# Kernel optimization log

Hardware: AMD Instinct MI355X
Metric: run time of the kernel (lower is better)

Reference implementation:

```python
import jax, jax.numpy as jnp
import numpy as np

B, HG, WG, D, NH, K = 4, 32, 32, 768, 12, 7
HD = D // NH  # 64


def _neigh_idx(H, W, k):
    # NATTEN semantics: 7x7 window centered at the query, shifted (clamped)
    # at borders so every query has exactly k*k neighbors.
    si = np.clip(np.arange(H) - k // 2, 0, H - k)  # [H] window row starts
    sj = np.clip(np.arange(W) - k // 2, 0, W - k)  # [W] window col starts
    ri = si[:, None] + np.arange(k)[None, :]       # [H, k]
    cj = sj[:, None] + np.arange(k)[None, :]       # [W, k]
    idx = ri[:, None, :, None] * W + cj[None, :, None, :]  # [H, W, k, k]
    return jnp.asarray(idx.reshape(H * W, k * k), dtype=jnp.int32)


def setup_inputs() -> dict:
    key = jax.random.key(0)
    ks = jax.random.split(key, 3)
    s = D ** -0.5
    return {
        "x": jax.random.normal(ks[0], (B, HG * WG, D), dtype=jnp.float32),
        "qkv_w": jax.random.normal(ks[1], (3 * D, D), dtype=jnp.float32) * s,
        "qkv_b": jnp.zeros((3 * D,), dtype=jnp.float32),
        "proj_w": jax.random.normal(ks[2], (D, D), dtype=jnp.float32) * s,
        "proj_b": jnp.zeros((D,), dtype=jnp.float32),
    }


def reference(x, qkv_w, qkv_b, proj_w, proj_b):
    b, n, d = x.shape  # n == HG*WG
    idx = _neigh_idx(HG, WG, K)  # [n, K*K] flat neighbor token indices

    qkv = x @ qkv_w.T + qkv_b                      # [b, n, 3d]
    q, k, v = jnp.split(qkv, 3, axis=-1)
    q = q.reshape(b, n, NH, HD) * (HD ** -0.5)     # [b, n, h, hd]
    k = k.reshape(b, n, NH, HD)
    v = v.reshape(b, n, NH, HD)

    kn = jnp.take(k, idx, axis=1)                  # [b, n, 49, h, hd]
    vn = jnp.take(v, idx, axis=1)                  # [b, n, 49, h, hd]

    scores = jnp.einsum('bnhd,bnkhd->bnhk', q, kn)  # [b, n, h, 49]
    attn = jax.nn.softmax(scores, axis=-1)
    out = jnp.einsum('bnhk,bnkhd->bnhd', attn, vn).reshape(b, n, d)
    return out @ proj_w.T + proj_b
```

## Files before the change

### kernel.cpp

```cpp
#include <hip/hip_runtime.h>


typedef __bf16 bf16x8 __attribute__((ext_vector_type(8)));
typedef short s16x4 __attribute__((ext_vector_type(4)));
typedef float f32x4 __attribute__((ext_vector_type(4)));

__device__ __forceinline__ unsigned short f2bf(float f) {
  unsigned u = __float_as_uint(f);
  u += 0x7fffu + ((u >> 16) & 1u);
  return (unsigned short)(u >> 16);
}

template <typename T>
__device__ __forceinline__ void gld_lds16(const T* g, T* l) {
  __builtin_amdgcn_global_load_lds((const __attribute__((address_space(1))) void*)g,
                                   (__attribute__((address_space(3))) void*)l, 16, 0, 0);
}

__global__ void cvt_kernel(const float* __restrict__ x, const float* __restrict__ w1,
                           const float* __restrict__ w2, unsigned short* __restrict__ xo,
                           unsigned short* __restrict__ w1o, unsigned short* __restrict__ w2o) {
  const int n1 = 4096 * 768 / 4;
  const int n2 = 2304 * 768 / 4;
  const int n3 = 768 * 768 / 4;
  int i = blockIdx.x * 256 + threadIdx.x;
  float4 v;
  unsigned short* dst;
  int o;
  if (i < n1) {
    o = i; v = ((const float4*)x)[o]; dst = xo;
  } else if (i < n1 + n2) {
    o = i - n1; v = ((const float4*)w1)[o]; dst = w1o;
  } else if (i < n1 + n2 + n3) {
    o = i - n1 - n2; v = ((const float4*)w2)[o]; dst = w2o;
  } else {
    return;
  }
  ushort4 r;
  r.x = f2bf(v.x); r.y = f2bf(v.y); r.z = f2bf(v.z); r.w = f2bf(v.w);
  ((ushort4*)dst)[o] = r;
}

template <int MT, int MODE>
__global__ __launch_bounds__(256) void gemm_bt(const unsigned short* __restrict__ A,
                                               const unsigned short* __restrict__ Bm,
                                               const float* __restrict__ bias,
                                               unsigned short* __restrict__ obf,
                                               unsigned short* __restrict__ vtout,
                                               float* __restrict__ of32,
                                               int M, int N, int Kd) {
  constexpr int BM = MT * 32;
  __shared__ __align__(16) unsigned short sA[2 * BM * 32];
  __shared__ __align__(16) unsigned short sB[2 * 128 * 32];
  const int tid = threadIdx.x;
  const int lane = tid & 63;
  const int wv = tid >> 6;
  const int m0 = blockIdx.y * BM, n0 = blockIdx.x * 128;
  const int wrow = (wv >> 1) * (MT * 16), wcol = (wv & 1) * 64;
  const int lr = lane & 15, lq = lane >> 4;

  f32x4 acc[MT][4] = {};

  const int ls = lane & 15, lc = lane >> 4;
  const unsigned short* pA  = A  + (size_t)(m0 + wv * 16 + ls) * Kd + lc * 8;
  const unsigned short* pA2 = A  + (size_t)(m0 + (wv + 4) * 16 + ls) * Kd + lc * 8;
  const unsigned short* pB  = Bm + (size_t)(n0 + wv * 16 + ls) * Kd + lc * 8;
  const unsigned short* pB2 = Bm + (size_t)(n0 + (wv + 4) * 16 + ls) * Kd + lc * 8;

  auto stage = [&](int it, int bsel) {
    const int k0 = it * 32;
    gld_lds16(pA + k0, sA + bsel * (BM * 32) + tid * 8);
    if (MT == 4) gld_lds16(pA2 + k0, sA + bsel * (BM * 32) + 2048 + tid * 8);
    gld_lds16(pB + k0, sB + bsel * 4096 + tid * 8);
    gld_lds16(pB2 + k0, sB + bsel * 4096 + 2048 + tid * 8);
  };

  const int nIter = Kd >> 5;
  stage(0, 0);
  __syncthreads();
  for (int it = 0; it < nIter; ++it) {
    const int cur = it & 1;
    if (it + 1 < nIter) stage(it + 1, cur ^ 1);
    const unsigned short* bA = sA + cur * (BM * 32);
    const unsigned short* bB = sB + cur * 4096;
    bf16x8 af[MT], bfr[4];
#pragma unroll
    for (int t = 0; t < MT; ++t)
      af[t] = *(const bf16x8*)(bA + ((wrow >> 4) + t) * 512 + lq * 128 + lr * 8);
#pragma unroll
    for (int t = 0; t < 4; ++t)
      bfr[t] = *(const bf16x8*)(bB + ((wcol >> 4) + t) * 512 + lq * 128 + lr * 8);
#pragma unroll
    for (int im = 0; im < MT; ++im)
#pragma unroll
      for (int in = 0; in < 4; ++in)
        acc[im][in] = __builtin_amdgcn_mfma_f32_16x16x32_bf16(af[im], bfr[in], acc[im][in], 0, 0, 0);
    __syncthreads();
  }

  if (MODE == 0) {
    const int sidx = n0 / 768;
    if (sidx == 2) {
#pragma unroll
      for (int im = 0; im < MT; ++im) {
#pragma unroll
        for (int in = 0; in < 4; ++in) {
          int gn = n0 + wcol + in * 16 + lr;
          int rem = gn - 1536;
          int hh = rem >> 6, dd = gn & 63;
          float bsv = bias[gn];
          int gm0 = m0 + wrow + im * 16 + lq * 4;
          ushort4 pk;
          pk.x = f2bf(acc[im][in][0] + bsv);
          pk.y = f2bf(acc[im][in][1] + bsv);
          pk.z = f2bf(acc[im][in][2] + bsv);
          pk.w = f2bf(acc[im][in][3] + bsv);
          *(ushort4*)(vtout + (size_t)(hh * 64 + dd) * 4096 + gm0) = pk;
        }
      }
    } else {
      const float scale = (sidx == 0) ? 0.18033688f : 1.0f;
#pragma unroll
      for (int im = 0; im < MT; ++im) {
#pragma unroll
        for (int in = 0; in < 4; ++in) {
          int gn = n0 + wcol + in * 16 + lr;
          int rem = gn - sidx * 768;
          int hh = rem >> 6, dd = gn & 63;
          float bsv = bias[gn];
#pragma unroll
          for (int r = 0; r < 4; ++r) {
            int gm = m0 + wrow + im * 16 + lq * 4 + r;
            float val = (acc[im][in][r] + bsv) * scale;
            obf[((size_t)(sidx * 12 + hh) * 4096 + gm) * 64 + dd] = f2bf(val);
          }
        }
      }
    }
  } else {
#pragma unroll
    for (int im = 0; im < MT; ++im) {
#pragma unroll
      for (int in = 0; in < 4; ++in) {
        int gn = n0 + wcol + in * 16 + lr;
        float bsv = bias[gn];
#pragma unroll
        for (int r = 0; r < 4; ++r) {
          int gm = m0 + wrow + im * 16 + lq * 4 + r;
          of32[(size_t)gm * N + gn] = acc[im][in][r] + bsv;
        }
      }
    }
  }
}

__global__ __launch_bounds__(256, 2) void natten_kernel(const unsigned short* __restrict__ qkvt,
                                                        unsigned short* __restrict__ aout) {
  __shared__ __align__(16) unsigned short sQ[64 * 64];
  __shared__ __align__(16) unsigned short sK[256 * 64];
  __shared__ __align__(16) unsigned short sVt[64 * 256];
  const int h = blockIdx.x, ip = blockIdx.y, b = blockIdx.z;
  const int i0 = ip * 2;
  const int tid = threadIdx.x, lane = tid & 63, wv = tid >> 6;
  const int lg = lane >> 4, lm = lane & 15;
  int si0 = i0 - 3; si0 = si0 < 0 ? 0 : si0; if (si0 > 25) si0 = 25;
  const int gb = b * 1024;
  const unsigned short* Qg = qkvt + ((size_t)h * 4096 + gb + i0 * 32) * 64;
  const unsigned short* Kg = qkvt + ((size_t)(12 + h) * 4096 + gb) * 64;
  const unsigned short* Vg = qkvt + (size_t)24 * 4096 * 64 + (size_t)h * 64 * 4096 + gb;

#pragma unroll
  for (int it = 0; it < 2; ++it) {
    int f = it * 256 + tid;
    int q = f >> 3, c16 = f & 7;
    uint4 v = *(const uint4*)(Qg + q * 64 + c16 * 8);
    int s = q & 15;
    *(uint2*)(sQ + q * 64 + ((((c16 << 1)) ^ s) << 2)) = make_uint2(v.x, v.y);
    *(uint2*)(sQ + q * 64 + ((((c16 << 1) | 1) ^ s) << 2)) = make_uint2(v.z, v.w);
  }
#pragma unroll
  for (int it = 0; it < 8; ++it) {
    int f = it * 256 + tid;
    int t = f >> 3, c16 = f & 7;
    int wr = t >> 5, c = t & 31;
    int row = si0 + wr; if (row > 31) row = 31;
    uint4 v = *(const uint4*)(Kg + (row * 32 + c) * 64 + c16 * 8);
    int s = t & 15;
    *(uint2*)(sK + t * 64 + ((((c16 << 1)) ^ s) << 2)) = make_uint2(v.x, v.y);
    *(uint2*)(sK + t * 64 + ((((c16 << 1) | 1) ^ s) << 2)) = make_uint2(v.z, v.w);
  }
#pragma unroll
  for (int it = 0; it < 8; ++it) {
    int f = it * 256 + tid;
    int d = f >> 5, tc16 = f & 31;
    int wr = tc16 >> 2;
    int row = si0 + wr; if (row > 31) row = 31;
    uint4 v = *(const uint4*)(Vg + (size_t)d * 4096 + row * 32 + (tc16 & 3) * 8);
    int s = d & 15;
    *(uint2*)(sVt + d * 256 + ((((tc16 << 1)) ^ s) << 2)) = make_uint2(v.x, v.y);
    *(uint2*)(sVt + d * 256 + ((((tc16 << 1) | 1) ^ s) << 2)) = make_uint2(v.z, v.w);
  }
  __syncthreads();

  const int row_sel = wv >> 1;
  const int jhalf = wv & 1;
  const int i = i0 + row_sel;
  int si_w = i - 3; si_w = si_w < 0 ? 0 : si_w; if (si_w > 25) si_w = 25;
  const int toff = (si_w - si0) * 32;
  const int j = jhalf * 16 + lm;
  int sj = j - 3; sj = sj < 0 ? 0 : sj; if (sj > 25) sj = 25;

  float madd[2][4];
#pragma unroll
  for (int p = 0; p < 2; ++p)
#pragma unroll
    for (int r = 0; r < 4; ++r) {
      int c = p * 16 + lg * 4 + r;
      madd[p][r] = (c >= sj && c <= sj + 6) ? 0.f : -1e30f;
    }

  s16x4 qf[4];
  const int qrow = row_sel * 32 + j;
#pragma unroll
  for (int ks = 0; ks < 4; ++ks)
    qf[ks] = *(const s16x4*)(sQ + qrow * 64 + ((((ks << 2) + lg) ^ (qrow & 15)) << 2));

  f32x4 accS[14];
#pragma unroll
  for (int tt = 0; tt < 14; ++tt) {
    f32x4 a = {0.f, 0.f, 0.f, 0.f};
    const int trow = toff + tt * 16 + lm;
    const unsigned short* kr = sK + trow * 64;
    const int sw = trow & 15;
#pragma unroll
    for (int ks = 0; ks < 4; ++ks) {
      s16x4 kf = *(const s16x4*)(kr + ((((ks << 2) + lg) ^ sw) << 2));
      a = __builtin_amdgcn_mfma_f32_16x16x16bf16_1k(kf, qf[ks], a, 0, 0, 0);
    }
    accS[tt] = a;
  }

  float mx = -3e38f;
#pragma unroll
  for (int tt = 0; tt < 14; ++tt)
#pragma unroll
    for (int r = 0; r < 4; ++r) {
      float v = accS[tt][r] + madd[tt & 1][r];
      accS[tt][r] = v;
      mx = fmaxf(mx, v);
    }
  mx = fmaxf(mx, __shfl_xor(mx, 16, 64));
  mx = fmaxf(mx, __shfl_xor(mx, 32, 64));
  float sum = 0.f;
#pragma unroll
  for (int tt = 0; tt < 14; ++tt)
#pragma unroll
    for (int r = 0; r < 4; ++r) {
      float p = exp2f(accS[tt][r] - mx);
      accS[tt][r] = p;
      sum += p;
    }
  sum += __shfl_xor(sum, 16, 64);
  sum += __shfl_xor(sum, 32, 64);
  const float inv = 1.f / sum;

  s16x4 pf[14];
#pragma unroll
  for (int tt = 0; tt < 14; ++tt) {
    union { unsigned u[2]; s16x4 v; } pk;
    pk.u[0] = ((unsigned)f2bf(accS[tt][1]) << 16) | f2bf(accS[tt][0]);
    pk.u[1] = ((unsigned)f2bf(accS[tt][3]) << 16) | f2bf(accS[tt][2]);
    pf[tt] = pk.v;
  }

  f32x4 accO[4] = {};
  const int choff = toff >> 2;
#pragma unroll
  for (int tt = 0; tt < 14; ++tt) {
    const int c8 = choff + tt * 4 + lg;
#pragma unroll
    for (int nt = 0; nt < 4; ++nt) {
      const int d = nt * 16 + lm;
      s16x4 vf = *(const s16x4*)(sVt + d * 256 + ((c8 ^ (d & 15)) << 2));
      accO[nt] = __builtin_amdgcn_mfma_f32_16x16x16bf16_1k(pf[tt], vf, accO[nt], 0, 0, 0);
    }
  }

  float invr[4];
#pragma unroll
  for (int r = 0; r < 4; ++r) invr[r] = __shfl(inv, lg * 4 + r, 64);

  const int tokbase = gb + i * 32 + jhalf * 16;
#pragma unroll
  for (int nt = 0; nt < 4; ++nt)
#pragma unroll
    for (int r = 0; r < 4; ++r) {
      int tok = tokbase + lg * 4 + r;
      aout[(size_t)tok * 768 + h * 64 + nt * 16 + lm] = f2bf(accO[nt][r] * invr[r]);
    }
}

extern "C" void kernel_launch(void* const* d_in, const int* in_sizes, int n_in,
                              void* d_out, int out_size, void* d_ws, size_t ws_size,
                              hipStream_t stream) {
  const float* x      = (const float*)d_in[0];
  const float* qkv_w  = (const float*)d_in[1];
  const float* qkv_b  = (const float*)d_in[2];
  const float* proj_w = (const float*)d_in[3];
  const float* proj_b = (const float*)d_in[4];
  char* ws = (char*)d_ws;

  unsigned short* xb    = (unsigned short*)(ws);
  unsigned short* wqkv  = (unsigned short*)(ws + 6291456);
  unsigned short* wproj = (unsigned short*)(ws + 9830400);
  unsigned short* qkvt  = (unsigned short*)(ws + 11010048);
  unsigned short* attnb = (unsigned short*)(ws + 29884416);
  unsigned short* vt    = qkvt + (size_t)24 * 4096 * 64;
  float* out = (float*)d_out;

  cvt_kernel<<<5376, 256, 0, stream>>>(x, qkv_w, proj_w, xb, wqkv, wproj);
  gemm_bt<4, 0><<<dim3(18, 32), 256, 0, stream>>>(xb, wqkv, qkv_b, qkvt, vt, nullptr, 4096, 2304, 768);
  natten_kernel<<<dim3(12, 16, 4), 256, 0, stream>>>(qkvt, attnb);
  gemm_bt<2, 1><<<dim3(6, 64), 256, 0, stream>>>(attnb, wproj, proj_b, nullptr, nullptr, out, 4096, 768, 768);
}
```

Baseline: 161.0 us.

## Load GEMM fragments directly from global into registers, dropping LDS staging

The bf16 GEMM no longer stages A and B tiles in shared memory through global_load_lds with double buffering and per-iteration barriers. Each wave now loads its own MFMA operand fragments straight from global memory into two register sets, alternating between them, with the K loop fully unrolled for a fixed K of 768. This removes LDS traffic and __syncthreads, and frees LDS, which may allow more waves per CU. The cost is that tiles which waves used to share are now fetched redundantly and rely on L1/L2 hits. The 16-byte per-lane reads along strided rows are also less coalesced, and the unrolled loop raises register pressure.

```diff
diff --git a/kernel.cpp b/kernel.cpp
--- a/kernel.cpp
+++ b/kernel.cpp
@@ -9,12 +9,6 @@
   unsigned u = __float_as_uint(f);
   u += 0x7fffu + ((u >> 16) & 1u);
   return (unsigned short)(u >> 16);
-}
-
-template <typename T>
-__device__ __forceinline__ void gld_lds16(const T* g, T* l) {
-  __builtin_amdgcn_global_load_lds((const __attribute__((address_space(1))) void*)g,
-                                   (__attribute__((address_space(3))) void*)l, 16, 0, 0);
 }
 
 __global__ void cvt_kernel(const float* __restrict__ x, const float* __restrict__ w1,
@@ -48,55 +42,54 @@
                                                unsigned short* __restrict__ obf,
                                                unsigned short* __restrict__ vtout,
                                                float* __restrict__ of32,
-                                               int M, int N, int Kd) {
-  constexpr int BM = MT * 32;
-  __shared__ __align__(16) unsigned short sA[2 * BM * 32];
-  __shared__ __align__(16) unsigned short sB[2 * 128 * 32];
-  const int tid = threadIdx.x;
-  const int lane = tid & 63;
-  const int wv = tid >> 6;
-  const int m0 = blockIdx.y * BM, n0 = blockIdx.x * 128;
-  const int wrow = (wv >> 1) * (MT * 16), wcol = (wv & 1) * 64;
+                                               int M, int N) {
+  constexpr int KD = 768;
+  const int tid = threadIdx.x, lane = tid & 63, wv = tid >> 6;
   const int lr = lane & 15, lq = lane >> 4;
+  const int m0 = blockIdx.y * (MT * 32) + (wv >> 1) * (MT * 16);
+  const int n0 = blockIdx.x * 128 + (wv & 1) * 64;
+
+  const unsigned short* pA[MT];
+  const unsigned short* pB[4];
+#pragma unroll
+  for (int t = 0; t < MT; ++t) pA[t] = A + (size_t)(m0 + t * 16 + lr) * KD + lq * 8;
+#pragma unroll
+  for (int t = 0; t < 4; ++t) pB[t] = Bm + (size_t)(n0 + t * 16 + lr) * KD + lq * 8;
 
   f32x4 acc[MT][4] = {};
-
-  const int ls = lane & 15, lc = lane >> 4;
-  const unsigned short* pA  = A  + (size_t)(m0 + wv * 16 + ls) * Kd + lc * 8;
-  const unsigned short* pA2 = A  + (size_t)(m0 + (wv + 4) * 16 + ls) * Kd + lc * 8;
-  const unsigned short* pB  = Bm + (size_t)(n0 + wv * 16 + ls) * Kd + lc * 8;
-  const unsigned short* pB2 = Bm + (size_t)(n0 + (wv + 4) * 16 + ls) * Kd + lc * 8;
-
-  auto stage = [&](int it, int bsel) {
-    const int k0 = it * 32;
-    gld_lds16(pA + k0, sA + bsel * (BM * 32) + tid * 8);
-    if (MT == 4) gld_lds16(pA2 + k0, sA + bsel * (BM * 32) + 2048 + tid * 8);
-    gld_lds16(pB + k0, sB + bsel * 4096 + tid * 8);
-    gld_lds16(pB2 + k0, sB + bsel * 4096 + 2048 + tid * 8);
+  bf16x8 a0[MT], b0[4], a1[MT], b1[4];
+
+  auto ldA = [&](bf16x8* d, int k) {
+#pragma unroll
+    for (int t = 0; t < MT; ++t) d[t] = *(const bf16x8*)(pA[t] + k);
   };
-
-  const int nIter = Kd >> 5;
-  stage(0, 0);
-  __syncthreads();
-  for (int it = 0; it < nIter; ++it) {
-    const int cur = it & 1;
-    if (it + 1 < nIter) stage(it + 1, cur ^ 1);
-    const unsigned short* bA = sA + cur * (BM * 32);
-    const unsigned short* bB = sB + cur * 4096;
-    bf16x8 af[MT], bfr[4];
-#pragma unroll
-    for (int t = 0; t < MT; ++t)
-      af[t] = *(const bf16x8*)(bA + ((wrow >> 4) + t) * 512 + lq * 128 + lr * 8);
-#pragma unroll
-    for (int t = 0; t < 4; ++t)
-      bfr[t] = *(const bf16x8*)(bB + ((wcol >> 4) + t) * 512 + lq * 128 + lr * 8);
+  auto ldB = [&](bf16x8* d, int k) {
+#pragma unroll
+    for (int t = 0; t < 4; ++t) d[t] = *(const bf16x8*)(pB[t] + k);
+  };
+  auto step = [&](bf16x8* a, bf16x8* b) {
 #pragma unroll
     for (int im = 0; im < MT; ++im)
 #pragma unroll
       for (int in = 0; in < 4; ++in)
-        acc[im][in] = __builtin_amdgcn_mfma_f32_16x16x32_bf16(af[im], bfr[in], acc[im][in], 0, 0, 0);
-    __syncthreads();
-  }
+        acc[im][in] = __builtin_amdgcn_mfma_f32_16x16x32_bf16(a[im], b[in], acc[im][in], 0, 0, 0);
+  };
+
+  ldA(a0, 0);
+  ldB(b0, 0);
+#pragma unroll
+  for (int k = 0; k < KD - 64; k += 64) {
+    ldA(a1, k + 32);
+    ldB(b1, k + 32);
+    step(a0, b0);
+    ldA(a0, k + 64);
+    ldB(b0, k + 64);
+    step(a1, b1);
+  }
+  ldA(a1, KD - 32);
+  ldB(b1, KD - 32);
+  step(a0, b0);
+  step(a1, b1);
 
   if (MODE == 0) {
     const int sidx = n0 / 768;
@@ -105,11 +98,11 @@
       for (int im = 0; im < MT; ++im) {
 #pragma unroll
         for (int in = 0; in < 4; ++in) {
-          int gn = n0 + wcol + in * 16 + lr;
+          int gn = n0 + in * 16 + lr;
           int rem = gn - 1536;
           int hh = rem >> 6, dd = gn & 63;
           float bsv = bias[gn];
-          int gm0 = m0 + wrow + im * 16 + lq * 4;
+          int gm0 = m0 + im * 16 + lq * 4;
           ushort4 pk;
           pk.x = f2bf(acc[im][in][0] + bsv);
           pk.y = f2bf(acc[im][in][1] + bsv);
@@ -124,13 +117,13 @@
       for (int im = 0; im < MT; ++im) {
 #pragma unroll
         for (int in = 0; in < 4; ++in) {
-          int gn = n0 + wcol + in * 16 + lr;
+          int gn = n0 + in * 16 + lr;
           int rem = gn - sidx * 768;
           int hh = rem >> 6, dd = gn & 63;
           float bsv = bias[gn];
 #pragma unroll
           for (int r = 0; r < 4; ++r) {
-            int gm = m0 + wrow + im * 16 + lq * 4 + r;
+            int gm = m0 + im * 16 + lq * 4 + r;
             float val = (acc[im][in][r] + bsv) * scale;
             obf[((size_t)(sidx * 12 + hh) * 4096 + gm) * 64 + dd] = f2bf(val);
           }
@@ -142,11 +135,11 @@
     for (int im = 0; im < MT; ++im) {
 #pragma unroll
       for (int in = 0; in < 4; ++in) {
-        int gn = n0 + wcol + in * 16 + lr;
+        int gn = n0 + in * 16 + lr;
         float bsv = bias[gn];
 #pragma unroll
         for (int r = 0; r < 4; ++r) {
-          int gm = m0 + wrow + im * 16 + lq * 4 + r;
+          int gm = m0 + im * 16 + lq * 4 + r;
           of32[(size_t)gm * N + gn] = acc[im][in][r] + bsv;
         }
       }
@@ -319,7 +312,7 @@
   float* out = (float*)d_out;
 
   cvt_kernel<<<5376, 256, 0, stream>>>(x, qkv_w, proj_w, xb, wqkv, wproj);
-  gemm_bt<4, 0><<<dim3(18, 32), 256, 0, stream>>>(xb, wqkv, qkv_b, qkvt, vt, nullptr, 4096, 2304, 768);
+  gemm_bt<4, 0><<<dim3(18, 32), 256, 0, stream>>>(xb, wqkv, qkv_b, qkvt, vt, nullptr, 4096, 2304);
   natten_kernel<<<dim3(12, 16, 4), 256, 0, stream>>>(qkvt, attnb);
-  gemm_bt<2, 1><<<dim3(6, 64), 256, 0, stream>>>(attnb, wproj, proj_b, nullptr, nullptr, out, 4096, 768, 768);
-}
+  gemm_bt<2, 1><<<dim3(6, 64), 256, 0, stream>>>(attnb, wproj, proj_b, nullptr, nullptr, out, 4096, 768);
+}
```

New measurement: 193.3 us. 20.0% more time.
